# Performance work log

Hardware: AMD Instinct MI355X
Metric: run time of the kernel (lower is better)

The kernel has to match this reference:

```python
import jax, jax.numpy as jnp
import numpy as np

LOSS1_COEFF = 1.0
LOSS2_COEFF = 1.0
LOSS3_COEFF = 1.0
LOSS4_COEFF = 0.5


def smooth_l1(x, y):
    # torch smooth_l1_loss, beta=1, reduction='mean'
    d = jnp.abs(x - y)
    return jnp.mean(jnp.where(d < 1.0, 0.5 * d * d, d - 0.5))


def setup_inputs() -> dict:
    key = jax.random.key(0)
    k1, k2 = jax.random.split(key)
    B, N, F = 256, 8192, 13
    targets = jax.random.uniform(k1, (B, N, F), dtype=jnp.float32)
    preds = jax.random.uniform(k2, (B, N, F), dtype=jnp.float32)
    return {"targets": targets, "preds": preds}


def reference(targets, preds):
    tb = targets[:, :, :4]  # [B,N,4]
    pb = preds[:, :, :4]
    # The original builds a [B,N,N] pairwise IoU matrix and takes its diagonal;
    # the diagonal is exactly the elementwise matched-pair IoU, computed here directly.
    xx1 = jnp.maximum(tb[..., 0], pb[..., 0])
    yy1 = jnp.maximum(tb[..., 1], pb[..., 1])
    xx2 = jnp.minimum(tb[..., 2], pb[..., 2])
    yy2 = jnp.minimum(tb[..., 3], pb[..., 3])
    w = jnp.clip(xx2 - xx1, 0.0)
    h = jnp.clip(yy2 - yy1, 0.0)
    inter = w * h
    area1 = (tb[..., 2] - tb[..., 0]) * (tb[..., 3] - tb[..., 1])
    area2 = (pb[..., 2] - pb[..., 0]) * (pb[..., 3] - pb[..., 1])
    ious = inter / (area1 + area2 - inter + 1e-07)  # [B,N]

    loss1 = smooth_l1(jnp.ones_like(ious), ious)
    loss2 = smooth_l1(tb, pb)
    loss3 = smooth_l1(targets[:, :, -1], preds[:, :, -1])
    loss4 = smooth_l1(targets[:, :, 4:12], preds[:, :, 4:12])
    return (LOSS1_COEFF * loss1 + LOSS2_COEFF * loss2
            + LOSS3_COEFF * loss3 + LOSS4_COEFF * loss4)
```

## Files before the change

### kernel.cpp

```cpp
#include <hip/hip_runtime.h>


#define NGRP   32768
#define GBYTES 3328
#define GFLOAT 832
#define NBUF   2
#define NBLK   512
#define NWAVE  (NBLK * 4)
#define GPW    (NGRP / NWAVE)

typedef const __attribute__((address_space(1))) float gfloat;
typedef __attribute__((address_space(3))) float lfloat;

__device__ __forceinline__ float sl1(float d) {
    d = fabsf(d);
    return d < 1.0f ? 0.5f * d * d : d - 0.5f;
}

__global__ __launch_bounds__(256) void loss_stage1(const float* __restrict__ T,
                                                   const float* __restrict__ P,
                                                   float* __restrict__ partial) {
    __shared__ float lds[4][NBUF][2][GFLOAT];
    __shared__ float wred[4];

    const int tid  = threadIdx.x;
    const int lane = tid & 63;
    const int wv   = tid >> 6;
    const int wid  = blockIdx.x * 4 + wv;

    auto stage = [&](int g, int b) {
        const char* tb = (const char*)T + (long long)g * GBYTES;
        const char* pb = (const char*)P + (long long)g * GBYTES;
        lfloat* lt = (lfloat*)&lds[wv][b][0][0];
        lfloat* lp = (lfloat*)&lds[wv][b][1][0];
#pragma unroll
        for (int s = 0; s < 3; ++s) {
            __builtin_amdgcn_global_load_lds((gfloat*)(tb + s * 1024 + lane * 16),
                                             lt + s * 256 + lane * 4, 16, 0, 0);
            __builtin_amdgcn_global_load_lds((gfloat*)(pb + s * 1024 + lane * 16),
                                             lp + s * 256 + lane * 4, 16, 0, 0);
        }
        __builtin_amdgcn_global_load_lds((gfloat*)(tb + 3072 + lane * 4),
                                         lt + 768 + lane, 4, 0, 0);
        __builtin_amdgcn_global_load_lds((gfloat*)(pb + 3072 + lane * 4),
                                         lp + 768 + lane, 4, 0, 0);
    };

    stage(wid, 0);
    stage(wid + NWAVE, 1);

    float acc = 0.0f;

    for (int i = 0; i < GPW; ++i) {
        if (i < GPW - 1) asm volatile("s_waitcnt vmcnt(8)" ::: "memory");
        else             asm volatile("s_waitcnt vmcnt(0)" ::: "memory");
        __builtin_amdgcn_sched_barrier(0);

        const int buf = i & 1;
        const float* t = &lds[wv][buf][0][0];
        const float* p = &lds[wv][buf][1][0];
        const int rb = lane * 13;

        float t0 = t[rb + 0], t1 = t[rb + 1], t2 = t[rb + 2], t3 = t[rb + 3];
        float p0 = p[rb + 0], p1 = p[rb + 1], p2 = p[rb + 2], p3 = p[rb + 3];

        float s2 = sl1(t0 - p0) + sl1(t1 - p1) + sl1(t2 - p2) + sl1(t3 - p3);

        float s4 = 0.0f;
#pragma unroll
        for (int f = 4; f < 12; ++f) s4 += sl1(t[rb + f] - p[rb + f]);

        float s3 = sl1(t[rb + 12] - p[rb + 12]);

        float xx1 = fmaxf(t0, p0);
        float yy1 = fmaxf(t1, p1);
        float xx2 = fminf(t2, p2);
        float yy2 = fminf(t3, p3);
        float w  = fmaxf(xx2 - xx1, 0.0f);
        float h  = fmaxf(yy2 - yy1, 0.0f);
        float inter = w * h;
        float a1 = (t2 - t0) * (t3 - t1);
        float a2 = (p2 - p0) * (p3 - p1);
        float iou = inter / (a1 + a2 - inter + 1e-7f);
        float s1 = sl1(1.0f - iou);

        constexpr float W1 = 1.0f / 2097152.0f;
        constexpr float W2 = 1.0f / 8388608.0f;
        constexpr float W3 = 1.0f / 2097152.0f;
        constexpr float W4 = 1.0f / 33554432.0f;
        acc += W1 * s1 + W2 * s2 + W3 * s3 + W4 * s4;

        if (i + 2 < GPW) stage(wid + (i + 2) * NWAVE, buf);
    }

#pragma unroll
    for (int off = 32; off > 0; off >>= 1)
        acc += __shfl_down(acc, off, 64);
    if (lane == 0) wred[wv] = acc;
    __syncthreads();
    if (tid == 0)
        partial[blockIdx.x] = wred[0] + wred[1] + wred[2] + wred[3];
}

__global__ __launch_bounds__(256) void loss_stage2(const float* __restrict__ partial,
                                                   float* __restrict__ out) {
    __shared__ float wred[4];
    const int tid = threadIdx.x;
    float a = 0.0f;
    for (int i = tid; i < NBLK; i += 256) a += partial[i];
#pragma unroll
    for (int off = 32; off > 0; off >>= 1)
        a += __shfl_down(a, off, 64);
    if ((tid & 63) == 0) wred[tid >> 6] = a;
    __syncthreads();
    if (tid == 0) out[0] = wred[0] + wred[1] + wred[2] + wred[3];
}

extern "C" void kernel_launch(void* const* d_in, const int* in_sizes, int n_in,
                              void* d_out, int out_size, void* d_ws, size_t ws_size,
                              hipStream_t stream) {
    const float* targets = (const float*)d_in[0];
    const float* preds   = (const float*)d_in[1];
    float* out     = (float*)d_out;
    float* partial = (float*)d_ws;

    loss_stage1<<<NBLK, 256, 0, stream>>>(targets, preds, partial);
    loss_stage2<<<1, 256, 0, stream>>>(partial, out);
}
```

Measured before the change: 227.5 us.

## Stage groups through registers instead of direct global-to-LDS loads

Replaces the asynchronous global_load_lds staging with ordinary vector global loads into registers. The registers are then written to a double-buffered LDS area and the compute reads from there. The main loop is unrolled by two with register prefetch running about two groups ahead, and explicit lgkmcnt waits replace the hand-tuned vmcnt waits. This aims to avoid the overhead or serialization of direct-to-LDS loads, at the cost of more VGPRs and extra LDS write instructions. The compiler-inserted vmcnt waits may also limit how many loads stay in flight.

```diff
diff --git a/kernel.cpp b/kernel.cpp
--- a/kernel.cpp
+++ b/kernel.cpp
@@ -4,93 +4,113 @@
 #define NGRP   32768
 #define GBYTES 3328
 #define GFLOAT 832
-#define NBUF   2
 #define NBLK   512
 #define NWAVE  (NBLK * 4)
 #define GPW    (NGRP / NWAVE)
 
-typedef const __attribute__((address_space(1))) float gfloat;
-typedef __attribute__((address_space(3))) float lfloat;
+struct Grp {
+    float4 t[3]; float tt;
+    float4 p[3]; float pt;
+};
 
 __device__ __forceinline__ float sl1(float d) {
     d = fabsf(d);
     return d < 1.0f ? 0.5f * d * d : d - 0.5f;
 }
 
+__device__ __forceinline__ void load_grp(const float* __restrict__ T,
+                                         const float* __restrict__ P,
+                                         long long g, int lane, Grp& r) {
+    const char* tb = (const char*)T + g * GBYTES;
+    const char* pb = (const char*)P + g * GBYTES;
+#pragma unroll
+    for (int s = 0; s < 3; ++s) {
+        r.t[s] = *(const float4*)(tb + s * 1024 + lane * 16);
+        r.p[s] = *(const float4*)(pb + s * 1024 + lane * 16);
+    }
+    r.tt = *(const float*)(tb + 3072 + lane * 4);
+    r.pt = *(const float*)(pb + 3072 + lane * 4);
+}
+
+__device__ __forceinline__ void write_grp(float* lt, float* lp, int lane, const Grp& r) {
+#pragma unroll
+    for (int s = 0; s < 3; ++s) {
+        *(float4*)((char*)lt + s * 1024 + lane * 16) = r.t[s];
+        *(float4*)((char*)lp + s * 1024 + lane * 16) = r.p[s];
+    }
+    lt[768 + lane] = r.tt;
+    lp[768 + lane] = r.pt;
+}
+
+__device__ __forceinline__ float compute_grp(const float* t, const float* p, int lane) {
+    const int rb = lane * 13;
+
+    float t0 = t[rb + 0], t1 = t[rb + 1], t2 = t[rb + 2], t3 = t[rb + 3];
+    float p0 = p[rb + 0], p1 = p[rb + 1], p2 = p[rb + 2], p3 = p[rb + 3];
+
+    float s2 = sl1(t0 - p0) + sl1(t1 - p1) + sl1(t2 - p2) + sl1(t3 - p3);
+
+    float s4 = 0.0f;
+#pragma unroll
+    for (int f = 4; f < 12; ++f) s4 += sl1(t[rb + f] - p[rb + f]);
+
+    float s3 = sl1(t[rb + 12] - p[rb + 12]);
+
+    float xx1 = fmaxf(t0, p0);
+    float yy1 = fmaxf(t1, p1);
+    float xx2 = fminf(t2, p2);
+    float yy2 = fminf(t3, p3);
+    float w  = fmaxf(xx2 - xx1, 0.0f);
+    float h  = fmaxf(yy2 - yy1, 0.0f);
+    float inter = w * h;
+    float a1 = (t2 - t0) * (t3 - t1);
+    float a2 = (p2 - p0) * (p3 - p1);
+    float iou = inter / (a1 + a2 - inter + 1e-7f);
+    float s1 = sl1(1.0f - iou);
+
+    constexpr float W1 = 1.0f / 2097152.0f;
+    constexpr float W2 = 1.0f / 8388608.0f;
+    constexpr float W3 = 1.0f / 2097152.0f;
+    constexpr float W4 = 1.0f / 33554432.0f;
+    return W1 * s1 + W2 * s2 + W3 * s3 + W4 * s4;
+}
+
 __global__ __launch_bounds__(256) void loss_stage1(const float* __restrict__ T,
                                                    const float* __restrict__ P,
                                                    float* __restrict__ partial) {
-    __shared__ float lds[4][NBUF][2][GFLOAT];
+    __shared__ __align__(16) float lds[4][2][2][GFLOAT];
     __shared__ float wred[4];
 
     const int tid  = threadIdx.x;
     const int lane = tid & 63;
     const int wv   = tid >> 6;
-    const int wid  = blockIdx.x * 4 + wv;
+    const long long wid = blockIdx.x * 4 + wv;
 
-    auto stage = [&](int g, int b) {
-        const char* tb = (const char*)T + (long long)g * GBYTES;
-        const char* pb = (const char*)P + (long long)g * GBYTES;
-        lfloat* lt = (lfloat*)&lds[wv][b][0][0];
-        lfloat* lp = (lfloat*)&lds[wv][b][1][0];
-#pragma unroll
-        for (int s = 0; s < 3; ++s) {
-            __builtin_amdgcn_global_load_lds((gfloat*)(tb + s * 1024 + lane * 16),
-                                             lt + s * 256 + lane * 4, 16, 0, 0);
-            __builtin_amdgcn_global_load_lds((gfloat*)(pb + s * 1024 + lane * 16),
-                                             lp + s * 256 + lane * 4, 16, 0, 0);
-        }
-        __builtin_amdgcn_global_load_lds((gfloat*)(tb + 3072 + lane * 4),
-                                         lt + 768 + lane, 4, 0, 0);
-        __builtin_amdgcn_global_load_lds((gfloat*)(pb + 3072 + lane * 4),
-                                         lp + 768 + lane, 4, 0, 0);
-    };
+    float* lt0 = &lds[wv][0][0][0];
+    float* lp0 = &lds[wv][0][1][0];
+    float* lt1 = &lds[wv][1][0][0];
+    float* lp1 = &lds[wv][1][1][0];
 
-    stage(wid, 0);
-    stage(wid + NWAVE, 1);
+    Grp r0, r1;
+    load_grp(T, P, wid, lane, r0);
+    load_grp(T, P, wid + NWAVE, lane, r1);
+    write_grp(lt0, lp0, lane, r0);
+    load_grp(T, P, wid + 2 * NWAVE, lane, r0);
 
     float acc = 0.0f;
 
-    for (int i = 0; i < GPW; ++i) {
-        if (i < GPW - 1) asm volatile("s_waitcnt vmcnt(8)" ::: "memory");
-        else             asm volatile("s_waitcnt vmcnt(0)" ::: "memory");
+    for (int i = 0; i < GPW; i += 2) {
+        asm volatile("s_waitcnt lgkmcnt(0)" ::: "memory");
         __builtin_amdgcn_sched_barrier(0);
+        acc += compute_grp(lt0, lp0, lane);
+        write_grp(lt1, lp1, lane, r1);
+        if (i + 3 < GPW) load_grp(T, P, wid + (long long)(i + 3) * NWAVE, lane, r1);
 
-        const int buf = i & 1;
-        const float* t = &lds[wv][buf][0][0];
-        const float* p = &lds[wv][buf][1][0];
-        const int rb = lane * 13;
-
-        float t0 = t[rb + 0], t1 = t[rb + 1], t2 = t[rb + 2], t3 = t[rb + 3];
-        float p0 = p[rb + 0], p1 = p[rb + 1], p2 = p[rb + 2], p3 = p[rb + 3];
-
-        float s2 = sl1(t0 - p0) + sl1(t1 - p1) + sl1(t2 - p2) + sl1(t3 - p3);
-
-        float s4 = 0.0f;
-#pragma unroll
-        for (int f = 4; f < 12; ++f) s4 += sl1(t[rb + f] - p[rb + f]);
-
-        float s3 = sl1(t[rb + 12] - p[rb + 12]);
-
-        float xx1 = fmaxf(t0, p0);
-        float yy1 = fmaxf(t1, p1);
-        float xx2 = fminf(t2, p2);
-        float yy2 = fminf(t3, p3);
-        float w  = fmaxf(xx2 - xx1, 0.0f);
-        float h  = fmaxf(yy2 - yy1, 0.0f);
-        float inter = w * h;
-        float a1 = (t2 - t0) * (t3 - t1);
-        float a2 = (p2 - p0) * (p3 - p1);
-        float iou = inter / (a1 + a2 - inter + 1e-7f);
-        float s1 = sl1(1.0f - iou);
-
-        constexpr float W1 = 1.0f / 2097152.0f;
-        constexpr float W2 = 1.0f / 8388608.0f;
-        constexpr float W3 = 1.0f / 2097152.0f;
-        constexpr float W4 = 1.0f / 33554432.0f;
-        acc += W1 * s1 + W2 * s2 + W3 * s3 + W4 * s4;
-
-        if (i + 2 < GPW) stage(wid + (i + 2) * NWAVE, buf);
+        asm volatile("s_waitcnt lgkmcnt(0)" ::: "memory");
+        __builtin_amdgcn_sched_barrier(0);
+        acc += compute_grp(lt1, lp1, lane);
+        if (i + 2 < GPW) write_grp(lt0, lp0, lane, r0);
+        if (i + 4 < GPW) load_grp(T, P, wid + (long long)(i + 4) * NWAVE, lane, r0);
     }
 
 #pragma unroll
```

New measurement: 238.5 us. +4.8%, slower.
